# Kernel optimization log

Measured on AMD Instinct MI355X. Metric: run time of the kernel, lower is better.

Reference implementation:

```python
import jax, jax.numpy as jnp
import numpy as np

EPS = 1e-3


def interpolate_dim(x, n_out):
    # linear interpolation along axis 1, align_corners=True (matches F.interpolate linear)
    n_in = x.shape[1]
    pos = jnp.linspace(0.0, n_in - 1.0, n_out)
    idx0 = jnp.floor(pos).astype(jnp.int32)
    idx1 = jnp.minimum(idx0 + 1, n_in - 1)
    w = (pos - idx0.astype(x.dtype))[None, :, None]
    return x[:, idx0] * (1.0 - w) + x[:, idx1] * w


def logits_to_a_coeff(a_logits, eps):
    # stability-triangle parameterization: |a1| < 2, |a1| - 1 < a2 < 1
    stab = 1.0 - eps
    a1 = 2.0 * jnp.tanh(a_logits[..., 0]) * stab
    a1_abs = jnp.abs(a1)
    a2 = 0.5 * ((2.0 - a1_abs) * jnp.tanh(a_logits[..., 1]) * stab + a1_abs)
    return jnp.stack([a1, a2], axis=-1)  # (B, T, 2)


def sample_wise_lpc(x, a_coeff):
    # time-varying all-pole: y[t] = x[t] - a1[t]*y[t-1] - a2[t]*y[t-2]
    bs = x.shape[0]
    xs = (x.T, a_coeff[..., 0].T, a_coeff[..., 1].T)  # (T, B) each

    def step(carry, inp):
        y1, y2 = carry
        xt, a1, a2 = inp
        y = xt - a1 * y1 - a2 * y2
        return (y, y1), y

    zero = jnp.zeros((bs,), x.dtype)
    _, ys = jax.lax.scan(step, (zero, zero), xs)
    return ys.T  # (B, T)


def time_varying_fir(y, b_coeff):
    # y_out[t] = b0[t]*y[t] + b1[t]*y[t-1] + b2[t]*y[t-2], zero initial conditions
    y_pad = jnp.pad(y, ((0, 0), (2, 0)))
    return (b_coeff[..., 0] * y
            + b_coeff[..., 1] * y_pad[:, 1:-1]
            + b_coeff[..., 2] * y_pad[:, :-2])


def setup_inputs() -> dict:
    key = jax.random.key(0)
    k1, k2 = jax.random.split(key)
    x = jax.random.normal(k1, (32, 262144), dtype=jnp.float32)
    coeff_logits = jax.random.normal(k2, (32, 256, 5), dtype=jnp.float32)
    return {"x": x, "coeff_logits": coeff_logits}


def reference(x, coeff_logits):
    n_samples = x.shape[1]
    # interp_coeff=False: interpolate logits to sample rate first
    logits = interpolate_dim(coeff_logits, n_samples)  # (B, n_samples, 5)
    a_coeff = logits_to_a_coeff(logits[..., :2], EPS)  # (B, n_samples, 2)
    b_coeff = logits[..., 2:]                          # (B, n_samples, 3)
    y_a = sample_wise_lpc(x, a_coeff)
    y_ab = time_varying_fir(y_a, b_coeff)
    return y_ab
```

## Files before the change

### kernel.cpp

```cpp
#include <hip/hip_runtime.h>
#include <math.h>

#define BATCH 32
#define NSAMP 262144
#define NKNOT 256
#define EPSV  0.001f
#define CH    16
#define CPB   256
#define NCROW (NSAMP / CH)
#define BPR   (NCROW / CPB)
#define NB    (BATCH * BPR)
#define NWAVE (CPB / 64)

__device__ __forceinline__ float fast_tanh(float x) {
    float e = __expf(2.0f * x);
    float r = __builtin_amdgcn_rcpf(e + 1.0f);
    return fmaf(-2.0f, r, 1.0f);
}

__global__ __launch_bounds__(256, 4) void k_agg(
    const float* __restrict__ x,
    const float* __restrict__ cl,
    float* __restrict__ G)
{
    __shared__ float wag[NWAVE][6];
    const int tid = threadIdx.x;
    const int b = blockIdx.x;
    const int lane = tid & 63, wid = tid >> 6;

    int chunk = b * CPB + tid;
    const float4* xp = (const float4*)(x + (size_t)chunk * CH);
    float xr[CH];
    *(float4*)&xr[0]  = xp[0];
    *(float4*)&xr[4]  = xp[1];
    *(float4*)&xr[8]  = xp[2];
    *(float4*)&xr[12] = xp[3];

    int r = chunk >> 14;
    int c = chunk & (NCROW - 1);
    const float scale = 255.0f / 262143.0f;
    float pos0 = (float)(c * CH) * scale;
    float fiA = floorf(pos0);
    int idxA = (int)fiA;
    float w0v = pos0 - fiA;
    const float* kb = cl + (size_t)r * NKNOT * 5;
    int i1 = min(idxA + 1, NKNOT - 1);
    int i2 = min(idxA + 2, NKNOT - 1);
    float k00 = kb[idxA*5+0], k01 = kb[i1*5+0], k02 = kb[i2*5+0];
    float k10 = kb[idxA*5+1], k11 = kb[i1*5+1], k12 = kb[i2*5+1];
    float d0A = k01-k00, d0B = k02-k01;
    float d1A = k11-k10, d1B = k12-k11;

    const float stab = 1.0f - EPSV, stab2 = 2.0f * stab;
    float p1 = 0.f, p2 = 0.f, A1 = 1.f, A2 = 0.f, B1 = 0.f, B2 = 1.f;
    #pragma unroll
    for (int j = 0; j < CH; ++j) {
        float w = fmaf((float)j, scale, w0v);
        bool sel = w >= 1.0f;
        float wu = sel ? w - 1.0f : w;
        float l0 = fmaf(wu, sel ? d0B : d0A, sel ? k01 : k00);
        float l1 = fmaf(wu, sel ? d1B : d1A, sel ? k11 : k10);
        float a1 = stab2 * fast_tanh(l0);
        float a1a = fabsf(a1);
        float a2 = 0.5f * fmaf((2.0f - a1a) * stab, fast_tanh(l1), a1a);
        float p  = fmaf(-a2, p2, xr[j]);  p = fmaf(-a1, p1, p);
        float hA = fmaf(-a1, A1, -a2 * A2);
        float hB = fmaf(-a1, B1, -a2 * B2);
        p2 = p1; p1 = p;
        A2 = A1; A1 = hA;
        B2 = B1; B1 = hB;
    }
    float L00 = A1, L01 = B1, L10 = A2, L11 = B2, Lv0 = p1, Lv1 = p2;

    #pragma unroll
    for (int d = 1; d < 64; d <<= 1) {
        float o00 = __shfl_up(L00, d), o01 = __shfl_up(L01, d);
        float o10 = __shfl_up(L10, d), o11 = __shfl_up(L11, d);
        float ov0 = __shfl_up(Lv0, d), ov1 = __shfl_up(Lv1, d);
        if (lane >= d) {
            float n00 = L00 * o00 + L01 * o10;
            float n01 = L00 * o01 + L01 * o11;
            float n10 = L10 * o00 + L11 * o10;
            float n11 = L10 * o01 + L11 * o11;
            float nv0 = fmaf(L00, ov0, fmaf(L01, ov1, Lv0));
            float nv1 = fmaf(L10, ov0, fmaf(L11, ov1, Lv1));
            L00 = n00; L01 = n01; L10 = n10; L11 = n11; Lv0 = nv0; Lv1 = nv1;
        }
    }
    if (lane == 63) {
        wag[wid][0] = L00; wag[wid][1] = L01; wag[wid][2] = L10;
        wag[wid][3] = L11; wag[wid][4] = Lv0; wag[wid][5] = Lv1;
    }
    __syncthreads();

    if (tid == CPB - 1) {
        float P00 = 1.f, P01 = 0.f, P10 = 0.f, P11 = 1.f, Pv0 = 0.f, Pv1 = 0.f;
        for (int w2 = 0; w2 < NWAVE - 1; ++w2) {
            float a00 = wag[w2][0], a01 = wag[w2][1], a10 = wag[w2][2];
            float a11 = wag[w2][3], av0 = wag[w2][4], av1 = wag[w2][5];
            float n00 = a00 * P00 + a01 * P10;
            float n01 = a00 * P01 + a01 * P11;
            float n10 = a10 * P00 + a11 * P10;
            float n11 = a10 * P01 + a11 * P11;
            float nv0 = fmaf(a00, Pv0, fmaf(a01, Pv1, av0));
            float nv1 = fmaf(a10, Pv0, fmaf(a11, Pv1, av1));
            P00 = n00; P01 = n01; P10 = n10; P11 = n11; Pv0 = nv0; Pv1 = nv1;
        }
        G[0*NB + b] = L00 * P00 + L01 * P10;
        G[1*NB + b] = L00 * P01 + L01 * P11;
        G[2*NB + b] = L10 * P00 + L11 * P10;
        G[3*NB + b] = L10 * P01 + L11 * P11;
        G[4*NB + b] = fmaf(L00, Pv0, fmaf(L01, Pv1, Lv0));
        G[5*NB + b] = fmaf(L10, Pv0, fmaf(L11, Pv1, Lv1));
    }
}

__global__ __launch_bounds__(256, 4) void k_apply(
    const float* __restrict__ x,
    const float* __restrict__ cl,
    const float* __restrict__ G,
    float* __restrict__ out)
{
    __shared__ float wag[NWAVE][6];
    __shared__ float sInit[2];
    const int tid = threadIdx.x;
    const int b = blockIdx.x;
    const int lane = tid & 63, wid = tid >> 6;

    if (wid == 0) {
        int rowFirst = b & ~(BPR - 1);
        int k = rowFirst + lane;
        float A00 = G[0*NB + k], A01 = G[1*NB + k], A10 = G[2*NB + k];
        float A11 = G[3*NB + k], Av0 = G[4*NB + k], Av1 = G[5*NB + k];
        #pragma unroll
        for (int d = 1; d < 64; d <<= 1) {
            float o00 = __shfl_up(A00, d), o01 = __shfl_up(A01, d);
            float o10 = __shfl_up(A10, d), o11 = __shfl_up(A11, d);
            float ov0 = __shfl_up(Av0, d), ov1 = __shfl_up(Av1, d);
            if (lane >= d) {
                float n00 = A00 * o00 + A01 * o10;
                float n01 = A00 * o01 + A01 * o11;
                float n10 = A10 * o00 + A11 * o10;
                float n11 = A10 * o01 + A11 * o11;
                float nv0 = fmaf(A00, ov0, fmaf(A01, ov1, Av0));
                float nv1 = fmaf(A10, ov0, fmaf(A11, ov1, Av1));
                A00 = n00; A01 = n01; A10 = n10; A11 = n11; Av0 = nv0; Av1 = nv1;
            }
        }
        int myIdx = b & (BPR - 1);
        int src = (myIdx > 0) ? myIdx - 1 : 0;
        float s0 = __shfl(Av0, src);
        float s1 = __shfl(Av1, src);
        if (lane == 0) {
            sInit[0] = myIdx ? s0 : 0.f;
            sInit[1] = myIdx ? s1 : 0.f;
        }
    }

    int chunk = b * CPB + tid;
    const float4* xp = (const float4*)(x + (size_t)chunk * CH);
    float xr[CH];
    *(float4*)&xr[0]  = xp[0];
    *(float4*)&xr[4]  = xp[1];
    *(float4*)&xr[8]  = xp[2];
    *(float4*)&xr[12] = xp[3];

    int r = chunk >> 14;
    int c = chunk & (NCROW - 1);
    const float scale = 255.0f / 262143.0f;
    float pos0 = (float)(c * CH) * scale;
    float fiA = floorf(pos0);
    int idxA = (int)fiA;
    float w0v = pos0 - fiA;
    const float* kb = cl + (size_t)r * NKNOT * 5;
    int i1 = min(idxA + 1, NKNOT - 1);
    int i2 = min(idxA + 2, NKNOT - 1);
    float k00 = kb[idxA*5+0], k01 = kb[i1*5+0], k02 = kb[i2*5+0];
    float k10 = kb[idxA*5+1], k11 = kb[i1*5+1], k12 = kb[i2*5+1];
    float k20 = kb[idxA*5+2], k21 = kb[i1*5+2], k22 = kb[i2*5+2];
    float k30 = kb[idxA*5+3], k31 = kb[i1*5+3], k32 = kb[i2*5+3];
    float k40 = kb[idxA*5+4], k41 = kb[i1*5+4], k42 = kb[i2*5+4];
    float d0A = k01-k00, d0B = k02-k01;
    float d1A = k11-k10, d1B = k12-k11;
    float d2A = k21-k20, d2B = k22-k21;
    float d3A = k31-k30, d3B = k32-k31;
    float d4A = k41-k40, d4B = k42-k41;

    const float stab = 1.0f - EPSV, stab2 = 2.0f * stab;
    float p1 = 0.f, p2 = 0.f, A1 = 1.f, A2 = 0.f, B1 = 0.f, B2 = 1.f;
    #pragma unroll
    for (int j = 0; j < CH; ++j) {
        float w = fmaf((float)j, scale, w0v);
        bool sel = w >= 1.0f;
        float wu = sel ? w - 1.0f : w;
        float l0 = fmaf(wu, sel ? d0B : d0A, sel ? k01 : k00);
        float l1 = fmaf(wu, sel ? d1B : d1A, sel ? k11 : k10);
        float a1 = stab2 * fast_tanh(l0);
        float a1a = fabsf(a1);
        float a2 = 0.5f * fmaf((2.0f - a1a) * stab, fast_tanh(l1), a1a);
        float p  = fmaf(-a2, p2, xr[j]);  p = fmaf(-a1, p1, p);
        float hA = fmaf(-a1, A1, -a2 * A2);
        float hB = fmaf(-a1, B1, -a2 * B2);
        p2 = p1; p1 = p;
        A2 = A1; A1 = hA;
        B2 = B1; B1 = hB;
    }
    float L00 = A1, L01 = B1, L10 = A2, L11 = B2, Lv0 = p1, Lv1 = p2;

    #pragma unroll
    for (int d = 1; d < 64; d <<= 1) {
        float o00 = __shfl_up(L00, d), o01 = __shfl_up(L01, d);
        float o10 = __shfl_up(L10, d), o11 = __shfl_up(L11, d);
        float ov0 = __shfl_up(Lv0, d), ov1 = __shfl_up(Lv1, d);
        if (lane >= d) {
            float n00 = L00 * o00 + L01 * o10;
            float n01 = L00 * o01 + L01 * o11;
            float n10 = L10 * o00 + L11 * o10;
            float n11 = L10 * o01 + L11 * o11;
            float nv0 = fmaf(L00, ov0, fmaf(L01, ov1, Lv0));
            float nv1 = fmaf(L10, ov0, fmaf(L11, ov1, Lv1));
            L00 = n00; L01 = n01; L10 = n10; L11 = n11; Lv0 = nv0; Lv1 = nv1;
        }
    }
    if (lane == 63) {
        wag[wid][0] = L00; wag[wid][1] = L01; wag[wid][2] = L10;
        wag[wid][3] = L11; wag[wid][4] = Lv0; wag[wid][5] = Lv1;
    }
    __syncthreads();
    float P00 = 1.f, P01 = 0.f, P10 = 0.f, P11 = 1.f, Pv0 = 0.f, Pv1 = 0.f;
    for (int w2 = 0; w2 < wid; ++w2) {
        float a00 = wag[w2][0], a01 = wag[w2][1], a10 = wag[w2][2];
        float a11 = wag[w2][3], av0 = wag[w2][4], av1 = wag[w2][5];
        float n00 = a00 * P00 + a01 * P10;
        float n01 = a00 * P01 + a01 * P11;
        float n10 = a10 * P00 + a11 * P10;
        float n11 = a10 * P01 + a11 * P11;
        float nv0 = fmaf(a00, Pv0, fmaf(a01, Pv1, av0));
        float nv1 = fmaf(a10, Pv0, fmaf(a11, Pv1, av1));
        P00 = n00; P01 = n01; P10 = n10; P11 = n11; Pv0 = nv0; Pv1 = nv1;
    }
    float E00 = __shfl_up(L00, 1), E01 = __shfl_up(L01, 1);
    float E10 = __shfl_up(L10, 1), E11 = __shfl_up(L11, 1);
    float Ev0 = __shfl_up(Lv0, 1), Ev1 = __shfl_up(Lv1, 1);
    if (lane == 0) { E00 = 1.f; E01 = 0.f; E10 = 0.f; E11 = 1.f; Ev0 = 0.f; Ev1 = 0.f; }
    float C00 = E00 * P00 + E01 * P10;
    float C01 = E00 * P01 + E01 * P11;
    float C10 = E10 * P00 + E11 * P10;
    float C11 = E10 * P01 + E11 * P11;
    float Cv0 = fmaf(E00, Pv0, fmaf(E01, Pv1, Ev0));
    float Cv1 = fmaf(E10, Pv0, fmaf(E11, Pv1, Ev1));

    float s0 = sInit[0], s1 = sInit[1];
    float y1 = fmaf(C00, s0, fmaf(C01, s1, Cv0));
    float y2 = fmaf(C10, s0, fmaf(C11, s1, Cv1));

    #pragma unroll
    for (int j = 0; j < CH; ++j) {
        float w = fmaf((float)j, scale, w0v);
        bool sel = w >= 1.0f;
        float wu = sel ? w - 1.0f : w;
        float l0 = fmaf(wu, sel ? d0B : d0A, sel ? k01 : k00);
        float l1 = fmaf(wu, sel ? d1B : d1A, sel ? k11 : k10);
        float b0 = fmaf(wu, sel ? d2B : d2A, sel ? k21 : k20);
        float b1c= fmaf(wu, sel ? d3B : d3A, sel ? k31 : k30);
        float b2c= fmaf(wu, sel ? d4B : d4A, sel ? k41 : k40);
        float a1 = stab2 * fast_tanh(l0);
        float a1a = fabsf(a1);
        float a2 = 0.5f * fmaf((2.0f - a1a) * stab, fast_tanh(l1), a1a);
        float y = fmaf(-a2, y2, xr[j]);  y = fmaf(-a1, y1, y);
        xr[j] = fmaf(b0, y, fmaf(b1c, y1, b2c * y2));
        y2 = y1; y1 = y;
    }

    float4* op = (float4*)(out + (size_t)chunk * CH);
    op[0] = *(const float4*)&xr[0];
    op[1] = *(const float4*)&xr[4];
    op[2] = *(const float4*)&xr[8];
    op[3] = *(const float4*)&xr[12];
}

extern "C" void kernel_launch(void* const* d_in, const int* in_sizes, int n_in,
                              void* d_out, int out_size, void* d_ws, size_t ws_size,
                              hipStream_t stream) {
    const float* x  = (const float*)d_in[0];
    const float* cl = (const float*)d_in[1];
    float* out = (float*)d_out;
    float* G = (float*)d_ws;

    hipLaunchKernelGGL(k_agg,   dim3(NB), dim3(CPB), 0, stream, x, cl, G);
    hipLaunchKernelGGL(k_apply, dim3(NB), dim3(CPB), 0, stream, x, cl, G, out);
}
```

Before: 40.61 us.

## Store per-chunk carry transforms in k_agg and drop recomputation in k_apply

k_agg now computes each thread's intra-block prefix transform (the 2x2 matrix plus offset that maps the block's initial state to the chunk's initial state) and writes six floats per chunk to workspace. k_apply reads these values and no longer repeats the first-pass recurrence, wave scan and tanh evaluations. Both kernels stream x in float4 pieces instead of holding 16 registers, and k_apply raises its occupancy hint to 6. This trades roughly half of k_apply's transcendental and scan work for extra global traffic of 24 bytes per chunk written and read (about 12.6 MB each way), and it needs a larger workspace.

```diff
diff --git a/kernel.cpp b/kernel.cpp
--- a/kernel.cpp
+++ b/kernel.cpp
@@ -10,6 +10,7 @@
 #define NCROW (NSAMP / CH)
 #define BPR   (NCROW / CPB)
 #define NB    (BATCH * BPR)
+#define TC    (NB * CPB)
 #define NWAVE (CPB / 64)
 
 __device__ __forceinline__ float fast_tanh(float x) {
@@ -21,6 +22,7 @@
 __global__ __launch_bounds__(256, 4) void k_agg(
     const float* __restrict__ x,
     const float* __restrict__ cl,
+    float* __restrict__ Cb,
     float* __restrict__ G)
 {
     __shared__ float wag[NWAVE][6];
@@ -30,11 +32,6 @@
 
     int chunk = b * CPB + tid;
     const float4* xp = (const float4*)(x + (size_t)chunk * CH);
-    float xr[CH];
-    *(float4*)&xr[0]  = xp[0];
-    *(float4*)&xr[4]  = xp[1];
-    *(float4*)&xr[8]  = xp[2];
-    *(float4*)&xr[12] = xp[3];
 
     int r = chunk >> 14;
     int c = chunk & (NCROW - 1);
@@ -54,21 +51,26 @@
     const float stab = 1.0f - EPSV, stab2 = 2.0f * stab;
     float p1 = 0.f, p2 = 0.f, A1 = 1.f, A2 = 0.f, B1 = 0.f, B2 = 1.f;
     #pragma unroll
-    for (int j = 0; j < CH; ++j) {
-        float w = fmaf((float)j, scale, w0v);
-        bool sel = w >= 1.0f;
-        float wu = sel ? w - 1.0f : w;
-        float l0 = fmaf(wu, sel ? d0B : d0A, sel ? k01 : k00);
-        float l1 = fmaf(wu, sel ? d1B : d1A, sel ? k11 : k10);
-        float a1 = stab2 * fast_tanh(l0);
-        float a1a = fabsf(a1);
-        float a2 = 0.5f * fmaf((2.0f - a1a) * stab, fast_tanh(l1), a1a);
-        float p  = fmaf(-a2, p2, xr[j]);  p = fmaf(-a1, p1, p);
-        float hA = fmaf(-a1, A1, -a2 * A2);
-        float hB = fmaf(-a1, B1, -a2 * B2);
-        p2 = p1; p1 = p;
-        A2 = A1; A1 = hA;
-        B2 = B1; B1 = hB;
+    for (int v4 = 0; v4 < 4; ++v4) {
+        float4 xq = xp[v4];
+        #pragma unroll
+        for (int q = 0; q < 4; ++q) {
+            int j = v4 * 4 + q;
+            float w = fmaf((float)j, scale, w0v);
+            bool sel = w >= 1.0f;
+            float wu = sel ? w - 1.0f : w;
+            float l0 = fmaf(wu, sel ? d0B : d0A, sel ? k01 : k00);
+            float l1 = fmaf(wu, sel ? d1B : d1A, sel ? k11 : k10);
+            float a1 = stab2 * fast_tanh(l0);
+            float a1a = fabsf(a1);
+            float a2 = 0.5f * fmaf((2.0f - a1a) * stab, fast_tanh(l1), a1a);
+            float p  = fmaf(-a2, p2, (&xq.x)[q]);  p = fmaf(-a1, p1, p);
+            float hA = fmaf(-a1, A1, -a2 * A2);
+            float hB = fmaf(-a1, B1, -a2 * B2);
+            p2 = p1; p1 = p;
+            A2 = A1; A1 = hA;
+            B2 = B1; B1 = hB;
+        }
     }
     float L00 = A1, L01 = B1, L10 = A2, L11 = B2, Lv0 = p1, Lv1 = p2;
 
@@ -93,19 +95,30 @@
     }
     __syncthreads();
 
+    float P00 = 1.f, P01 = 0.f, P10 = 0.f, P11 = 1.f, Pv0 = 0.f, Pv1 = 0.f;
+    for (int w2 = 0; w2 < wid; ++w2) {
+        float a00 = wag[w2][0], a01 = wag[w2][1], a10 = wag[w2][2];
+        float a11 = wag[w2][3], av0 = wag[w2][4], av1 = wag[w2][5];
+        float n00 = a00 * P00 + a01 * P10;
+        float n01 = a00 * P01 + a01 * P11;
+        float n10 = a10 * P00 + a11 * P10;
+        float n11 = a10 * P01 + a11 * P11;
+        float nv0 = fmaf(a00, Pv0, fmaf(a01, Pv1, av0));
+        float nv1 = fmaf(a10, Pv0, fmaf(a11, Pv1, av1));
+        P00 = n00; P01 = n01; P10 = n10; P11 = n11; Pv0 = nv0; Pv1 = nv1;
+    }
+    float E00 = __shfl_up(L00, 1), E01 = __shfl_up(L01, 1);
+    float E10 = __shfl_up(L10, 1), E11 = __shfl_up(L11, 1);
+    float Ev0 = __shfl_up(Lv0, 1), Ev1 = __shfl_up(Lv1, 1);
+    if (lane == 0) { E00 = 1.f; E01 = 0.f; E10 = 0.f; E11 = 1.f; Ev0 = 0.f; Ev1 = 0.f; }
+    Cb[0*TC + chunk] = E00 * P00 + E01 * P10;
+    Cb[1*TC + chunk] = E00 * P01 + E01 * P11;
+    Cb[2*TC + chunk] = E10 * P00 + E11 * P10;
+    Cb[3*TC + chunk] = E10 * P01 + E11 * P11;
+    Cb[4*TC + chunk] = fmaf(E00, Pv0, fmaf(E01, Pv1, Ev0));
+    Cb[5*TC + chunk] = fmaf(E10, Pv0, fmaf(E11, Pv1, Ev1));
+
     if (tid == CPB - 1) {
-        float P00 = 1.f, P01 = 0.f, P10 = 0.f, P11 = 1.f, Pv0 = 0.f, Pv1 = 0.f;
-        for (int w2 = 0; w2 < NWAVE - 1; ++w2) {
-            float a00 = wag[w2][0], a01 = wag[w2][1], a10 = wag[w2][2];
-            float a11 = wag[w2][3], av0 = wag[w2][4], av1 = wag[w2][5];
-            float n00 = a00 * P00 + a01 * P10;
-            float n01 = a00 * P01 + a01 * P11;
-            float n10 = a10 * P00 + a11 * P10;
-            float n11 = a10 * P01 + a11 * P11;
-            float nv0 = fmaf(a00, Pv0, fmaf(a01, Pv1, av0));
-            float nv1 = fmaf(a10, Pv0, fmaf(a11, Pv1, av1));
-            P00 = n00; P01 = n01; P10 = n10; P11 = n11; Pv0 = nv0; Pv1 = nv1;
-        }
         G[0*NB + b] = L00 * P00 + L01 * P10;
         G[1*NB + b] = L00 * P01 + L01 * P11;
         G[2*NB + b] = L10 * P00 + L11 * P10;
@@ -115,13 +128,13 @@
     }
 }
 
-__global__ __launch_bounds__(256, 4) void k_apply(
+__global__ __launch_bounds__(256, 6) void k_apply(
     const float* __restrict__ x,
     const float* __restrict__ cl,
+    const float* __restrict__ Cb,
     const float* __restrict__ G,
     float* __restrict__ out)
 {
-    __shared__ float wag[NWAVE][6];
     __shared__ float sInit[2];
     const int tid = threadIdx.x;
     const int b = blockIdx.x;
@@ -158,13 +171,6 @@
     }
 
     int chunk = b * CPB + tid;
-    const float4* xp = (const float4*)(x + (size_t)chunk * CH);
-    float xr[CH];
-    *(float4*)&xr[0]  = xp[0];
-    *(float4*)&xr[4]  = xp[1];
-    *(float4*)&xr[8]  = xp[2];
-    *(float4*)&xr[12] = xp[3];
-
     int r = chunk >> 14;
     int c = chunk & (NCROW - 1);
     const float scale = 255.0f / 262143.0f;
@@ -186,97 +192,42 @@
     float d3A = k31-k30, d3B = k32-k31;
     float d4A = k41-k40, d4B = k42-k41;
 
-    const float stab = 1.0f - EPSV, stab2 = 2.0f * stab;
-    float p1 = 0.f, p2 = 0.f, A1 = 1.f, A2 = 0.f, B1 = 0.f, B2 = 1.f;
-    #pragma unroll
-    for (int j = 0; j < CH; ++j) {
-        float w = fmaf((float)j, scale, w0v);
-        bool sel = w >= 1.0f;
-        float wu = sel ? w - 1.0f : w;
-        float l0 = fmaf(wu, sel ? d0B : d0A, sel ? k01 : k00);
-        float l1 = fmaf(wu, sel ? d1B : d1A, sel ? k11 : k10);
-        float a1 = stab2 * fast_tanh(l0);
-        float a1a = fabsf(a1);
-        float a2 = 0.5f * fmaf((2.0f - a1a) * stab, fast_tanh(l1), a1a);
-        float p  = fmaf(-a2, p2, xr[j]);  p = fmaf(-a1, p1, p);
-        float hA = fmaf(-a1, A1, -a2 * A2);
-        float hB = fmaf(-a1, B1, -a2 * B2);
-        p2 = p1; p1 = p;
-        A2 = A1; A1 = hA;
-        B2 = B1; B1 = hB;
-    }
-    float L00 = A1, L01 = B1, L10 = A2, L11 = B2, Lv0 = p1, Lv1 = p2;
-
-    #pragma unroll
-    for (int d = 1; d < 64; d <<= 1) {
-        float o00 = __shfl_up(L00, d), o01 = __shfl_up(L01, d);
-        float o10 = __shfl_up(L10, d), o11 = __shfl_up(L11, d);
-        float ov0 = __shfl_up(Lv0, d), ov1 = __shfl_up(Lv1, d);
-        if (lane >= d) {
-            float n00 = L00 * o00 + L01 * o10;
-            float n01 = L00 * o01 + L01 * o11;
-            float n10 = L10 * o00 + L11 * o10;
-            float n11 = L10 * o01 + L11 * o11;
-            float nv0 = fmaf(L00, ov0, fmaf(L01, ov1, Lv0));
-            float nv1 = fmaf(L10, ov0, fmaf(L11, ov1, Lv1));
-            L00 = n00; L01 = n01; L10 = n10; L11 = n11; Lv0 = nv0; Lv1 = nv1;
-        }
-    }
-    if (lane == 63) {
-        wag[wid][0] = L00; wag[wid][1] = L01; wag[wid][2] = L10;
-        wag[wid][3] = L11; wag[wid][4] = Lv0; wag[wid][5] = Lv1;
-    }
+    float C00 = Cb[0*TC + chunk], C01 = Cb[1*TC + chunk];
+    float C10 = Cb[2*TC + chunk], C11 = Cb[3*TC + chunk];
+    float Cv0 = Cb[4*TC + chunk], Cv1 = Cb[5*TC + chunk];
+
     __syncthreads();
-    float P00 = 1.f, P01 = 0.f, P10 = 0.f, P11 = 1.f, Pv0 = 0.f, Pv1 = 0.f;
-    for (int w2 = 0; w2 < wid; ++w2) {
-        float a00 = wag[w2][0], a01 = wag[w2][1], a10 = wag[w2][2];
-        float a11 = wag[w2][3], av0 = wag[w2][4], av1 = wag[w2][5];
-        float n00 = a00 * P00 + a01 * P10;
-        float n01 = a00 * P01 + a01 * P11;
-        float n10 = a10 * P00 + a11 * P10;
-        float n11 = a10 * P01 + a11 * P11;
-        float nv0 = fmaf(a00, Pv0, fmaf(a01, Pv1, av0));
-        float nv1 = fmaf(a10, Pv0, fmaf(a11, Pv1, av1));
-        P00 = n00; P01 = n01; P10 = n10; P11 = n11; Pv0 = nv0; Pv1 = nv1;
-    }
-    float E00 = __shfl_up(L00, 1), E01 = __shfl_up(L01, 1);
-    float E10 = __shfl_up(L10, 1), E11 = __shfl_up(L11, 1);
-    float Ev0 = __shfl_up(Lv0, 1), Ev1 = __shfl_up(Lv1, 1);
-    if (lane == 0) { E00 = 1.f; E01 = 0.f; E10 = 0.f; E11 = 1.f; Ev0 = 0.f; Ev1 = 0.f; }
-    float C00 = E00 * P00 + E01 * P10;
-    float C01 = E00 * P01 + E01 * P11;
-    float C10 = E10 * P00 + E11 * P10;
-    float C11 = E10 * P01 + E11 * P11;
-    float Cv0 = fmaf(E00, Pv0, fmaf(E01, Pv1, Ev0));
-    float Cv1 = fmaf(E10, Pv0, fmaf(E11, Pv1, Ev1));
-
     float s0 = sInit[0], s1 = sInit[1];
     float y1 = fmaf(C00, s0, fmaf(C01, s1, Cv0));
     float y2 = fmaf(C10, s0, fmaf(C11, s1, Cv1));
 
+    const float stab = 1.0f - EPSV, stab2 = 2.0f * stab;
+    const float4* xp = (const float4*)(x + (size_t)chunk * CH);
+    float4* op = (float4*)(out + (size_t)chunk * CH);
     #pragma unroll
-    for (int j = 0; j < CH; ++j) {
-        float w = fmaf((float)j, scale, w0v);
-        bool sel = w >= 1.0f;
-        float wu = sel ? w - 1.0f : w;
-        float l0 = fmaf(wu, sel ? d0B : d0A, sel ? k01 : k00);
-        float l1 = fmaf(wu, sel ? d1B : d1A, sel ? k11 : k10);
-        float b0 = fmaf(wu, sel ? d2B : d2A, sel ? k21 : k20);
-        float b1c= fmaf(wu, sel ? d3B : d3A, sel ? k31 : k30);
-        float b2c= fmaf(wu, sel ? d4B : d4A, sel ? k41 : k40);
-        float a1 = stab2 * fast_tanh(l0);
-        float a1a = fabsf(a1);
-        float a2 = 0.5f * fmaf((2.0f - a1a) * stab, fast_tanh(l1), a1a);
-        float y = fmaf(-a2, y2, xr[j]);  y = fmaf(-a1, y1, y);
-        xr[j] = fmaf(b0, y, fmaf(b1c, y1, b2c * y2));
-        y2 = y1; y1 = y;
-    }
-
-    float4* op = (float4*)(out + (size_t)chunk * CH);
-    op[0] = *(const float4*)&xr[0];
-    op[1] = *(const float4*)&xr[4];
-    op[2] = *(const float4*)&xr[8];
-    op[3] = *(const float4*)&xr[12];
+    for (int v4 = 0; v4 < 4; ++v4) {
+        float4 xq = xp[v4];
+        float4 ov;
+        #pragma unroll
+        for (int q = 0; q < 4; ++q) {
+            int j = v4 * 4 + q;
+            float w = fmaf((float)j, scale, w0v);
+            bool sel = w >= 1.0f;
+            float wu = sel ? w - 1.0f : w;
+            float l0 = fmaf(wu, sel ? d0B : d0A, sel ? k01 : k00);
+            float l1 = fmaf(wu, sel ? d1B : d1A, sel ? k11 : k10);
+            float b0 = fmaf(wu, sel ? d2B : d2A, sel ? k21 : k20);
+            float b1c= fmaf(wu, sel ? d3B : d3A, sel ? k31 : k30);
+            float b2c= fmaf(wu, sel ? d4B : d4A, sel ? k41 : k40);
+            float a1 = stab2 * fast_tanh(l0);
+            float a1a = fabsf(a1);
+            float a2 = 0.5f * fmaf((2.0f - a1a) * stab, fast_tanh(l1), a1a);
+            float y = fmaf(-a2, y2, (&xq.x)[q]);  y = fmaf(-a1, y1, y);
+            (&ov.x)[q] = fmaf(b0, y, fmaf(b1c, y1, b2c * y2));
+            y2 = y1; y1 = y;
+        }
+        op[v4] = ov;
+    }
 }
 
 extern "C" void kernel_launch(void* const* d_in, const int* in_sizes, int n_in,
@@ -285,8 +236,9 @@
     const float* x  = (const float*)d_in[0];
     const float* cl = (const float*)d_in[1];
     float* out = (float*)d_out;
-    float* G = (float*)d_ws;
-
-    hipLaunchKernelGGL(k_agg,   dim3(NB), dim3(CPB), 0, stream, x, cl, G);
-    hipLaunchKernelGGL(k_apply, dim3(NB), dim3(CPB), 0, stream, x, cl, G, out);
-}
+    float* Cb = (float*)d_ws;
+    float* G  = Cb + (size_t)6 * TC;
+
+    hipLaunchKernelGGL(k_agg,   dim3(NB), dim3(CPB), 0, stream, x, cl, Cb, G);
+    hipLaunchKernelGGL(k_apply, dim3(NB), dim3(CPB), 0, stream, x, cl, Cb, G, out);
+}
```

New measurement: 38.95 us. 1.04x faster.
